# Optimization experiments

Hardware: AMD Instinct MI355X
Metric: run time of the kernel (lower is better)

The kernel has to match this reference:

```python
import jax, jax.numpy as jnp
import numpy as np

IN_FEATURES = 4096
OUT_FEATURES = 11008
GROUP_SIZE = 128
NUM_GROUPS = IN_FEATURES // GROUP_SIZE  # 32


def setup_inputs() -> dict:
    key = jax.random.key(0)
    k1, k2, k3, k4, k5 = jax.random.split(key, 5)
    x = jax.random.normal(k1, (4, 2048, IN_FEATURES), dtype=jnp.float32)
    # packed 4-bit weights: each int holds (high << 4) | low, values in [0, 256)
    qweight = jax.random.randint(k2, (IN_FEATURES // 2, OUT_FEATURES), 0, 256, dtype=jnp.int32)
    scales = jax.random.uniform(k3, (NUM_GROUPS, OUT_FEATURES), dtype=jnp.float32) * 0.01 + 1e-4
    zeros = jax.random.normal(k4, (NUM_GROUPS, OUT_FEATURES), dtype=jnp.float32) * 0.01
    bias = jax.random.normal(k5, (OUT_FEATURES,), dtype=jnp.float32) * 0.01
    return {"x": x, "qweight": qweight, "scales": scales, "zeros": zeros, "bias": bias}


def _dequantize(qweight, scales, zeros, dtype):
    # unpack two 4-bit values per byte; even input rows = low nibble, odd = high nibble
    low = ((qweight & 15) - 8).astype(dtype)          # [in/2, out]
    high = (((qweight >> 4) & 15) - 8).astype(dtype)  # [in/2, out]
    w = jnp.stack([low, high], axis=1).reshape(IN_FEATURES, OUT_FEATURES)
    # per-group affine dequant: w = q * scale + zero
    w = w.reshape(NUM_GROUPS, GROUP_SIZE, OUT_FEATURES)
    w = w * scales[:, None, :] + zeros[:, None, :]
    return w.reshape(IN_FEATURES, OUT_FEATURES)


def reference(x, qweight, scales, zeros, bias):
    weight = _dequantize(qweight, scales, zeros, x.dtype)  # [in, out]
    # F.linear(x, weight.T, bias) == x @ weight + bias
    return jnp.einsum('bsi,io->bso', x, weight) + bias
```

## Files before the change

kernel.cpp:

```cpp
#include <hip/hip_runtime.h>
#include <hip/hip_bf16.h>

#define IN_F 4096
#define OUT_F 11008
#define GSIZE 128
#define M_TOTAL 8192

typedef float f32x4 __attribute__((ext_vector_type(4)));
typedef float f32x16 __attribute__((ext_vector_type(16)));
typedef unsigned short u16x8 __attribute__((ext_vector_type(8)));
typedef unsigned int u32x4 __attribute__((ext_vector_type(4)));
typedef __bf16 bf16x8 __attribute__((ext_vector_type(8)));

#define ASG __attribute__((address_space(1)))
#define ASL __attribute__((address_space(3)))

__device__ __forceinline__ unsigned short f2bf(float f) {
    union { float f; unsigned int u; } v;
    v.f = f;
    unsigned int u = v.u;
    unsigned int r = (u + 0x7fffu + ((u >> 16) & 1u)) >> 16;
    return (unsigned short)r;
}


__global__ void convert_x_frag_kernel(const float* __restrict__ x,
                                      unsigned short* __restrict__ xb) {
    const int mf = blockIdx.x;
    const int r  = threadIdx.x >> 3;
    const int kb = (threadIdx.x & 7) * 8;
    const int k0 = blockIdx.y * 512;
    const float* src = x + (size_t)(mf * 32 + r) * IN_F;
    unsigned short* dst = xb + (size_t)mf * (IN_F / 16) * 512;
#pragma unroll
    for (int kk = 0; kk < 512; kk += 64) {
        const int k = k0 + kk + kb;
        f32x4 a = *(const f32x4*)(src + k);
        f32x4 b = *(const f32x4*)(src + k + 4);
        u16x8 v;
#pragma unroll
        for (int e = 0; e < 4; ++e) {
            v[e]     = f2bf(a[e]);
            v[e + 4] = f2bf(b[e]);
        }
        const int kf = k >> 4, q2 = (k >> 3) & 1;
        *(u16x8*)(dst + (size_t)kf * 512 + (q2 * 32 + r) * 8) = v;
    }
}

__global__ void dequant_w_frag_kernel(const int* __restrict__ qw,
                                      const float* __restrict__ scales,
                                      const float* __restrict__ zeros,
                                      unsigned short* __restrict__ wt) {
    const int n  = blockIdx.x * 256 + threadIdx.x;
    const int k0 = blockIdx.y * 32;
    const int g  = k0 >> 7;
    const float s = scales[(size_t)g * OUT_F + n];
    const float z = zeros[(size_t)g * OUT_F + n];

    unsigned short outv[32];
#pragma unroll
    for (int i = 0; i < 16; ++i) {
        int q = qw[(size_t)(k0 / 2 + i) * OUT_F + n];
        float lo = (float)((q & 15) - 8) * s + z;
        float hi = (float)(((q >> 4) & 15) - 8) * s + z;
        outv[2 * i]     = f2bf(lo);
        outv[2 * i + 1] = f2bf(hi);
    }
    const int nf = n >> 5, r32 = n & 31;
    unsigned short* base = wt + (size_t)nf * (IN_F / 16) * 512 +
                           (size_t)(k0 >> 4) * 512;
    const u16x8* sv = (const u16x8*)outv;
#pragma unroll
    for (int c = 0; c < 4; ++c)
        *(u16x8*)(base + (c >> 1) * 512 + ((c & 1) * 32 + r32) * 8) = sv[c];
}

__global__ void dequant_w_rowmajor_kernel(const int* __restrict__ qw,
                                          const float* __restrict__ scales,
                                          const float* __restrict__ zeros,
                                          unsigned short* __restrict__ wt) {
    const int n  = blockIdx.x * 256 + threadIdx.x;
    const int k0 = blockIdx.y * 32;
    const int g  = k0 >> 7;
    const float s = scales[(size_t)g * OUT_F + n];
    const float z = zeros[(size_t)g * OUT_F + n];

    unsigned short outv[32];
#pragma unroll
    for (int i = 0; i < 16; ++i) {
        int q = qw[(size_t)(k0 / 2 + i) * OUT_F + n];
        float lo = (float)((q & 15) - 8) * s + z;
        float hi = (float)(((q >> 4) & 15) - 8) * s + z;
        outv[2 * i]     = f2bf(lo);
        outv[2 * i + 1] = f2bf(hi);
    }
    u16x8* dst = (u16x8*)(wt + (size_t)n * IN_F + k0);
    const u16x8* src = (const u16x8*)outv;
#pragma unroll
    for (int i = 0; i < 4; ++i) dst[i] = src[i];
}

__global__ __launch_bounds__(512, 1)
void gemm_kc2(const unsigned short* __restrict__ xb,
              const unsigned short* __restrict__ wt,
              const float* __restrict__ bias,
              float* __restrict__ out) {
    constexpr int NT = IN_F / 64;
    constexpr int NKF = IN_F / 16;
    __shared__ __attribute__((aligned(128))) unsigned short lds[65536];

    const int bid = (int)blockIdx.x;
    const int xcd = bid & 7;
    const int l   = bid >> 3;
    const int m0 = (xcd * 4 + (l & 3)) * 256;
    const int n0 = (l >> 2) * 256;

    const int tid  = threadIdx.x;
    const int lane = tid & 63;
    const int wave = tid >> 6;
    const int wr = wave >> 2;
    const int wc = wave & 3;
    const int r32 = lane & 31;
    const int q2  = lane >> 5;

    const ASG char* xbc = (const ASG char*)xb;
    const ASG char* wtc = (const ASG char*)wt;
    ASL char* ldsc = (ASL char*)lds;

    const int mfb = m0 >> 5;
    const int nfb = n0 >> 5;
    unsigned int oA[4], oB[4];
    int dA[4], dB[4];
#pragma unroll
    for (int kc = 0; kc < 4; ++kc) {
        oA[kc] = (unsigned int)(((mfb + wave) * NKF + kc) * 1024 + lane * 16);
        oB[kc] = (unsigned int)(((nfb + wave) * NKF + kc) * 1024 + lane * 16);
        dA[kc] = (wave * 4 + kc) * 1024;
        dB[kc] = 32768 + (wave * 4 + kc) * 1024;
    }

#define STG_Z(KC, P)                                                           \
    do {                                                                       \
        __builtin_amdgcn_global_load_lds(                                      \
            (ASG const unsigned int*)(xbc + oA[(KC)]),                         \
            (ASL unsigned int*)(ldsc + dA[(KC)] + (P) * 65536), 16, 0, 0);     \
        __builtin_amdgcn_global_load_lds(                                      \
            (ASG const unsigned int*)(wtc + oB[(KC)]),                         \
            (ASL unsigned int*)(ldsc + dB[(KC)] + (P) * 65536), 16, 0, 0);     \
        oA[(KC)] += 4096;                                                      \
        oB[(KC)] += 4096;                                                      \
    } while (0)

#define BAR()                                                                  \
    do {                                                                       \
        __builtin_amdgcn_sched_barrier(0);                                     \
        __builtin_amdgcn_s_barrier();                                          \
        __builtin_amdgcn_sched_barrier(0);                                     \
    } while (0)

    bf16x8 afR[2][4];
    bf16x8 bfR[2][2];
    f32x16 acc[4][2];
#pragma unroll
    for (int i = 0; i < 4; ++i)
#pragma unroll
        for (int j = 0; j < 2; ++j) acc[i][j] = (f32x16)0.0f;

#define READ_KC(P, KC, S)                                                      \
    do {                                                                       \
        const unsigned short* _b = lds + (P) * 32768 + lane * 8;               \
        _Pragma("unroll") for (int _m = 0; _m < 4; ++_m)                       \
            afR[S][_m] = *(const bf16x8*)(_b +                                 \
                (((wr * 4 + _m) * 4 + (KC)) << 9));                            \
        _Pragma("unroll") for (int _n = 0; _n < 2; ++_n)                       \
            bfR[S][_n] = *(const bf16x8*)(_b + 16384 +                         \
                (((wc * 2 + _n) * 4 + (KC)) << 9));                            \
    } while (0)

#define QUAD_KC(S)                                                             \
    do {                                                                       \
        __builtin_amdgcn_s_setprio(1);                                         \
        _Pragma("unroll") for (int _m = 0; _m < 4; ++_m)                       \
        _Pragma("unroll") for (int _n = 0; _n < 2; ++_n)                       \
            acc[_m][_n] = __builtin_amdgcn_mfma_f32_32x32x16_bf16(             \
                afR[S][_m], bfR[S][_n], acc[_m][_n], 0, 0, 0);                 \
        __builtin_amdgcn_s_setprio(0);                                         \
    } while (0)

#pragma unroll
    for (int kc = 0; kc < 4; ++kc) STG_Z(kc, 0);
#pragma unroll
    for (int kc = 0; kc < 4; ++kc) STG_Z(kc, 1);
    __builtin_amdgcn_sched_barrier(0);
    asm volatile("s_waitcnt vmcnt(8)" ::: "memory");
    BAR();
    READ_KC(0, 0, 0);
    BAR();

#pragma unroll 1
    for (int tt = 0; tt < NT; tt += 2) {
        const bool g2 = (tt + 2 < NT);
        const bool g3 = (tt + 3 < NT);
        QUAD_KC(0); READ_KC(0, 1, 1); if (g2) STG_Z(0, 0); BAR();
        QUAD_KC(1); READ_KC(0, 2, 0); if (g2) STG_Z(1, 0); BAR();
        QUAD_KC(0); READ_KC(0, 3, 1); if (g2) STG_Z(2, 0);
        __builtin_amdgcn_sched_barrier(0);
        if (g2) {
            asm volatile("s_waitcnt vmcnt(6)" ::: "memory");
        } else {
            asm volatile("s_waitcnt vmcnt(0)" ::: "memory");
        }
        BAR();
        QUAD_KC(1);
        READ_KC(1, 0, 0);
        if (g2) STG_Z(3, 0);
        BAR();
        QUAD_KC(0); READ_KC(1, 1, 1); if (g3) STG_Z(0, 1); BAR();
        QUAD_KC(1); READ_KC(1, 2, 0); if (g3) STG_Z(1, 1); BAR();
        QUAD_KC(0); READ_KC(1, 3, 1); if (g3) STG_Z(2, 1);
        __builtin_amdgcn_sched_barrier(0);
        if (g3) {
            asm volatile("s_waitcnt vmcnt(6)" ::: "memory");
        } else {
            asm volatile("s_waitcnt vmcnt(0)" ::: "memory");
        }
        BAR();
        QUAD_KC(1);
        if (g2) READ_KC(0, 0, 0);
        if (g3) STG_Z(3, 1);
        BAR();
    }

#pragma unroll
    for (int nf = 0; nf < 2; ++nf) {
        const int col = n0 + wc * 64 + nf * 32 + r32;
        const float bv = bias[col];
#pragma unroll
        for (int mf = 0; mf < 4; ++mf) {
            const int row0 = m0 + wr * 128 + mf * 32 + q2 * 4;
#pragma unroll
            for (int r = 0; r < 16; ++r) {
                const int row = row0 + (r & 3) + ((r >> 2) << 3);
                __builtin_nontemporal_store(acc[mf][nf][r] + bv,
                                            &out[(size_t)row * OUT_F + col]);
            }
        }
    }
#undef STG_Z
#undef BAR
#undef READ_KC
#undef QUAD_KC
}

template <bool PREW>
__global__ __launch_bounds__(256, 2)
void gemm_kernel(const float* __restrict__ x,
                 const unsigned short* __restrict__ wt,
                 const int* __restrict__ qw,
                 const float* __restrict__ scales,
                 const float* __restrict__ zeros,
                 const float* __restrict__ bias,
                 float* __restrict__ out) {
    constexpr int BM = 128, BN = 128, BK = 64;
    constexpr int LDK = BK + 8;
    constexpr int NT = IN_F / BK;

    __shared__ unsigned short As[BM * LDK];
    __shared__ unsigned short Bs[BN * LDK];

    const int bid = blockIdx.x;
    constexpr int NB_N = OUT_F / BN;
    const int m0 = (bid / NB_N) * BM;
    const int n0 = (bid % NB_N) * BN;

    const int tid  = threadIdx.x;
    const int lane = tid & 63;
    const int wave = tid >> 6;
    const int wr = wave >> 1, wc = wave & 1;

    const int st_row = tid >> 3;
    const int st_col = (tid & 7) * 8;

    f32x4 areg[4][2];
    u32x4 breg[4];
    int   qreg[16];
    float s_, z_;
    const int b_n  = tid & 127;
    const int b_kp = (tid >> 7) * 16;

    auto load_tile = [&](int kt) {
        {
            const float* base = x + (size_t)m0 * IN_F + (size_t)kt * BK + st_col;
#pragma unroll
            for (int p = 0; p < 4; ++p) {
                const float* rp = base + (size_t)(p * 32 + st_row) * IN_F;
                areg[p][0] = *(const f32x4*)rp;
                areg[p][1] = *(const f32x4*)(rp + 4);
            }
        }
        if constexpr (PREW) {
            const unsigned short* base = wt + (size_t)n0 * IN_F + (size_t)kt * BK + st_col;
#pragma unroll
            for (int p = 0; p < 4; ++p)
                breg[p] = *(const u32x4*)(base + (size_t)(p * 32 + st_row) * IN_F);
        } else {
            const int kp0 = kt * (BK / 2) + b_kp;
#pragma unroll
            for (int i = 0; i < 16; ++i)
                qreg[i] = qw[(size_t)(kp0 + i) * OUT_F + n0 + b_n];
            const int g = (kt * BK) >> 7;
            s_ = scales[(size_t)g * OUT_F + n0 + b_n];
            z_ = zeros[(size_t)g * OUT_F + n0 + b_n];
        }
    };

    auto write_lds = [&]() {
#pragma unroll
        for (int p = 0; p < 4; ++p) {
            u16x8 v;
#pragma unroll
            for (int e = 0; e < 4; ++e) {
                v[e]     = f2bf(areg[p][0][e]);
                v[e + 4] = f2bf(areg[p][1][e]);
            }
            *(u16x8*)(&As[(p * 32 + st_row) * LDK + st_col]) = v;
        }
        if constexpr (PREW) {
#pragma unroll
            for (int p = 0; p < 4; ++p)
                *(u32x4*)(&Bs[(p * 32 + st_row) * LDK + st_col]) = breg[p];
        } else {
            unsigned short tmp[32];
#pragma unroll
            for (int i = 0; i < 16; ++i) {
                int q = qreg[i];
                tmp[2 * i]     = f2bf((float)((q & 15) - 8) * s_ + z_);
                tmp[2 * i + 1] = f2bf((float)(((q >> 4) & 15) - 8) * s_ + z_);
            }
            const u16x8* srcv = (const u16x8*)tmp;
#pragma unroll
            for (int i = 0; i < 4; ++i)
                *(u16x8*)(&Bs[b_n * LDK + 2 * b_kp + 8 * i]) = srcv[i];
        }
    };

    f32x4 acc[4][4];
#pragma unroll
    for (int i = 0; i < 4; ++i)
#pragma unroll
        for (int j = 0; j < 4; ++j) acc[i][j] = (f32x4)0.0f;

    load_tile(0);

#pragma unroll 1
    for (int kt = 0; kt < NT; ++kt) {
        __syncthreads();
        write_lds();
        __syncthreads();
        if (kt + 1 < NT) load_tile(kt + 1);

#pragma unroll
        for (int kk = 0; kk < 2; ++kk) {
            const int kidx = kk * 32 + ((lane >> 4) << 3);
            bf16x8 afv[4], bfv[4];
#pragma unroll
            for (int i = 0; i < 4; ++i)
                afv[i] = *(const bf16x8*)(&As[(wr * 64 + i * 16 + (lane & 15)) * LDK + kidx]);
#pragma unroll
            for (int j = 0; j < 4; ++j)
                bfv[j] = *(const bf16x8*)(&Bs[(wc * 64 + j * 16 + (lane & 15)) * LDK + kidx]);
#pragma unroll
            for (int i = 0; i < 4; ++i)
#pragma unroll
                for (int j = 0; j < 4; ++j)
                    acc[i][j] = __builtin_amdgcn_mfma_f32_16x16x32_bf16(afv[i], bfv[j], acc[i][j], 0, 0, 0);
        }
    }

    const int orow_base = m0 + wr * 64 + ((lane >> 4) << 2);
    const int ocol_base = n0 + wc * 64 + (lane & 15);
#pragma unroll
    for (int j = 0; j < 4; ++j) {
        const float bv = bias[ocol_base + j * 16];
#pragma unroll
        for (int i = 0; i < 4; ++i) {
#pragma unroll
            for (int q = 0; q < 4; ++q) {
                out[(size_t)(orow_base + i * 16 + q) * OUT_F + (ocol_base + j * 16)] =
                    acc[i][j][q] + bv;
            }
        }
    }
}

extern "C" void kernel_launch(void* const* d_in, const int* in_sizes, int n_in,
                              void* d_out, int out_size, void* d_ws, size_t ws_size,
                              hipStream_t stream) {
    const float* x      = (const float*)d_in[0];
    const int*   qw     = (const int*)d_in[1];
    const float* scales = (const float*)d_in[2];
    const float* zeros  = (const float*)d_in[3];
    const float* bias   = (const float*)d_in[4];
    float* out = (float*)d_out;

    const size_t wt_bytes = (size_t)OUT_F * IN_F * sizeof(unsigned short);
    const size_t xb_bytes = (size_t)M_TOTAL * IN_F * sizeof(unsigned short);

    if (ws_size >= wt_bytes + xb_bytes) {
        unsigned short* wt = (unsigned short*)d_ws;
        unsigned short* xb = (unsigned short*)((char*)d_ws + wt_bytes);
        convert_x_frag_kernel<<<dim3(M_TOTAL / 32, 8), 256, 0, stream>>>(x, xb);
        dequant_w_frag_kernel<<<dim3(OUT_F / 256, IN_F / 32), 256, 0, stream>>>(qw, scales, zeros, wt);
        gemm_kc2<<<(M_TOTAL / 256) * (OUT_F / 256), 512, 0, stream>>>(xb, wt, bias, out);
    } else if (ws_size >= wt_bytes) {
        unsigned short* wt = (unsigned short*)d_ws;
        dequant_w_rowmajor_kernel<<<dim3(OUT_F / 256, IN_F / 32), 256, 0, stream>>>(qw, scales, zeros, wt);
        gemm_kernel<true><<<(M_TOTAL / 128) * (OUT_F / 128), 256, 0, stream>>>(x, wt, qw, scales, zeros, bias, out);
    } else {
        gemm_kernel<false><<<(M_TOTAL / 128) * (OUT_F / 128), 256, 0, stream>>>(x, nullptr, qw, scales, zeros, bias, out);
    }
}
```

Measured before the change: 691.0 us.

## Halve barriers per K-tile in GEMM main loop by regrouping stage/read/MFMA

Reschedules the bf16 MFMA GEMM main loop so each barrier covers two MFMA quads instead of one. The global-to-LDS staging of the last chunk of the next buffer is deferred into the loop, and the vmcnt waits are adjusted to match. The goal is less workgroup-barrier overhead and longer uninterrupted MFMA runs. The trade-off is a tighter LDS reuse window, so the ordering has to stay correct for buffer hazards.

```diff
diff --git a/kernel.cpp b/kernel.cpp
--- a/kernel.cpp
+++ b/kernel.cpp
@@ -102,7 +102,7 @@
 }
 
 __global__ __launch_bounds__(512, 1)
-void gemm_kc2(const unsigned short* __restrict__ xb,
+void gemm_kc3(const unsigned short* __restrict__ xb,
               const unsigned short* __restrict__ wt,
               const float* __restrict__ bias,
               float* __restrict__ out) {
@@ -190,10 +190,9 @@
 
 #pragma unroll
     for (int kc = 0; kc < 4; ++kc) STG_Z(kc, 0);
-#pragma unroll
-    for (int kc = 0; kc < 4; ++kc) STG_Z(kc, 1);
+    STG_Z(0, 1); STG_Z(1, 1); STG_Z(2, 1);
     __builtin_amdgcn_sched_barrier(0);
-    asm volatile("s_waitcnt vmcnt(8)" ::: "memory");
+    asm volatile("s_waitcnt vmcnt(6)" ::: "memory");
     BAR();
     READ_KC(0, 0, 0);
     BAR();
@@ -202,33 +201,45 @@
     for (int tt = 0; tt < NT; tt += 2) {
         const bool g2 = (tt + 2 < NT);
         const bool g3 = (tt + 3 < NT);
-        QUAD_KC(0); READ_KC(0, 1, 1); if (g2) STG_Z(0, 0); BAR();
-        QUAD_KC(1); READ_KC(0, 2, 0); if (g2) STG_Z(1, 0); BAR();
-        QUAD_KC(0); READ_KC(0, 3, 1); if (g2) STG_Z(2, 0);
+        QUAD_KC(0);
+        READ_KC(0, 1, 1);
+        QUAD_KC(1);
+        READ_KC(0, 2, 0);
+        if (g2) STG_Z(0, 0);
+        STG_Z(3, 1);
+        BAR();
+        QUAD_KC(0);
+        READ_KC(0, 3, 1);
+        QUAD_KC(1);
+        if (g2) { STG_Z(1, 0); STG_Z(2, 0); }
         __builtin_amdgcn_sched_barrier(0);
         if (g2) {
-            asm volatile("s_waitcnt vmcnt(6)" ::: "memory");
+            asm volatile("s_waitcnt vmcnt(4)" ::: "memory");
         } else {
             asm volatile("s_waitcnt vmcnt(0)" ::: "memory");
         }
+        __builtin_amdgcn_sched_barrier(0);
+        READ_KC(1, 0, 0);
         BAR();
+        QUAD_KC(0);
+        READ_KC(1, 1, 1);
         QUAD_KC(1);
-        READ_KC(1, 0, 0);
+        READ_KC(1, 2, 0);
+        if (g3) STG_Z(0, 1);
         if (g2) STG_Z(3, 0);
         BAR();
-        QUAD_KC(0); READ_KC(1, 1, 1); if (g3) STG_Z(0, 1); BAR();
-        QUAD_KC(1); READ_KC(1, 2, 0); if (g3) STG_Z(1, 1); BAR();
-        QUAD_KC(0); READ_KC(1, 3, 1); if (g3) STG_Z(2, 1);
+        QUAD_KC(0);
+        READ_KC(1, 3, 1);
+        QUAD_KC(1);
+        if (g3) { STG_Z(1, 1); STG_Z(2, 1); }
         __builtin_amdgcn_sched_barrier(0);
         if (g3) {
-            asm volatile("s_waitcnt vmcnt(6)" ::: "memory");
+            asm volatile("s_waitcnt vmcnt(4)" ::: "memory");
         } else {
             asm volatile("s_waitcnt vmcnt(0)" ::: "memory");
         }
-        BAR();
-        QUAD_KC(1);
+        __builtin_amdgcn_sched_barrier(0);
         if (g2) READ_KC(0, 0, 0);
-        if (g3) STG_Z(3, 1);
         BAR();
     }
 
@@ -412,7 +423,7 @@
         unsigned short* xb = (unsigned short*)((char*)d_ws + wt_bytes);
         convert_x_frag_kernel<<<dim3(M_TOTAL / 32, 8), 256, 0, stream>>>(x, xb);
         dequant_w_frag_kernel<<<dim3(OUT_F / 256, IN_F / 32), 256, 0, stream>>>(qw, scales, zeros, wt);
-        gemm_kc2<<<(M_TOTAL / 256) * (OUT_F / 256), 512, 0, stream>>>(xb, wt, bias, out);
+        gemm_kc3<<<(M_TOTAL / 256) * (OUT_F / 256), 512, 0, stream>>>(xb, wt, bias, out);
     } else if (ws_size >= wt_bytes) {
         unsigned short* wt = (unsigned short*)d_ws;
         dequant_w_rowmajor_kernel<<<dim3(OUT_F / 256, IN_F / 32), 256, 0, stream>>>(qw, scales, zeros, wt);
```

After: 693.5 us. About the same (+0.4%).
